# Kernel tuning notes

Measured on AMD Instinct MI355X. Metric: run time of the kernel, lower is better.

## Reference

```python
import jax, jax.numpy as jnp
import numpy as np

C = 20        # class_num
B = 2         # boxes per cell, N = B*5 + C = 30
S = 7         # grid size
NB = 16384    # batch
LAMBDA_COORD = 5.0
LAMBDA_NOOBJ = 0.5
OBJ_P = 0.2


def setup_inputs() -> dict:
    key = jax.random.key(0)
    ks = jax.random.split(key, 8)
    pred = jax.random.uniform(ks[0], (NB, S, S, B * 5 + C), jnp.float32)
    # object indicator per cell (target conf channel must be exactly 1 for obj cells)
    obj = (jax.random.uniform(ks[1], (NB, S, S, 1)) < OBJ_P).astype(jnp.float32)
    parts = []
    for b in range(B):
        xy = jax.random.uniform(ks[2 + 2 * b], (NB, S, S, 2), jnp.float32)
        wh = jax.random.uniform(ks[3 + 2 * b], (NB, S, S, 2), jnp.float32) * 0.9 + 0.05
        parts += [xy, wh, obj]
    cls = jax.random.uniform(ks[6], (NB, S, S, C), jnp.float32)
    target = jnp.concatenate(parts + [cls], axis=-1)
    return {"pred_tensor": pred, "target_tensor": target}


def _yolo_loss(pred, target):
    Nb, Sg, _, N = pred.shape
    Bb = (N - C) // 5
    dt = pred.dtype
    # grid[..., 0] = column (x offset), grid[..., 1] = row (y offset)
    gx, gy = jnp.meshgrid(jnp.arange(Sg), jnp.arange(Sg), indexing="xy")
    grid = jnp.stack([gx, gy], axis=-1).astype(dt)          # [S,S,2]

    pb = pred[..., : 5 * Bb].reshape(Nb, Sg, Sg, Bb, 5)      # raw pred boxes [Nb,S,S,B,5]
    tb0 = target[..., :5]                                    # raw gt box 0  [Nb,S,S,5]

    # txty -> absolute xy (normalized by S); wh stays raw
    pxy = (pb[..., :2] + grid[None, :, :, None, :]) / Sg
    pwh = pb[..., 2:4]
    gxy = (tb0[..., :2] + grid[None]) / Sg
    gwh = tb0[..., 2:4]

    # corners
    p1, p2 = pxy - 0.5 * pwh, pxy + 0.5 * pwh                # [Nb,S,S,B,2]
    g1 = (gxy - 0.5 * gwh)[..., None, :]                     # [Nb,S,S,1,2]
    g2 = (gxy + 0.5 * gwh)[..., None, :]

    # IoU of gt box against each of the B pred boxes, per cell
    wh = jnp.clip(jnp.minimum(g2, p2) - jnp.maximum(g1, p1), 0.0)
    inter = wh[..., 0] * wh[..., 1]                          # [Nb,S,S,B]
    area_p = pwh[..., 0] * pwh[..., 1]
    area_g = (gwh[..., 0] * gwh[..., 1])[..., None]
    iou = inter / (area_g + area_p - inter)

    best = jnp.argmax(iou, axis=-1)                          # [Nb,S,S]
    best_iou = jax.lax.stop_gradient(jnp.max(iou, axis=-1))  # .item() in torch detaches
    best_box = jnp.take_along_axis(pb, best[..., None, None], axis=3)[..., 0, :]  # raw [Nb,S,S,5]

    obj = target[..., 4] == 1.0
    objf = obj.astype(dt)
    noobjf = (target[..., 4] < 1.0).astype(dt)

    # coord losses (responsible box only)
    loss_xy = LAMBDA_COORD * jnp.sum(objf[..., None] * (best_box[..., :2] - tb0[..., :2]) ** 2)
    gwh_safe = jnp.where(obj[..., None], gwh, 1.0)           # keep sqrt grads finite under mask
    pwh_safe = jnp.where(obj[..., None], jnp.clip(best_box[..., 2:4], 0.0, 1.0), 1.0)
    loss_wh = LAMBDA_COORD * jnp.sum(objf[..., None] * (jnp.sqrt(pwh_safe) - jnp.sqrt(gwh_safe)) ** 2)

    loss_conf_posi = jnp.sum(objf * (best_box[..., 4] - best_iou) ** 2)
    loss_class = jnp.sum(objf[..., None] * (pred[..., 5 * Bb:] - target[..., 5 * Bb:]) ** 2)

    # negative conf: all B confs in no-obj cells + non-best confs in obj cells
    conf_all = pb[..., 4]                                    # [Nb,S,S,B]
    onehot = jax.nn.one_hot(best, Bb, dtype=dt)
    neg_w = objf[..., None] * (1.0 - onehot) + noobjf[..., None]
    loss_conf_nega = LAMBDA_NOOBJ * jnp.sum(neg_w * conf_all ** 2)

    total = loss_xy + loss_wh + loss_conf_posi + loss_conf_nega + loss_class
    bs = jnp.asarray(Nb, dt)
    return total / bs / bs  # original divides by batch_size twice


def reference(pred_tensor, target_tensor):
    return _yolo_loss(pred_tensor, target_tensor)
```

## Files before the change

kernel.cpp:

```cpp
#include <hip/hip_runtime.h>
#include <math.h>

constexpr int NCH = 30;
constexpr int CLS = 20;
constexpr int CPB = 256;
constexpr int NTHREADS = 256;

__global__ __launch_bounds__(NTHREADS) void yolo_loss_main(
    const float* __restrict__ pred, const float* __restrict__ targ,
    float* __restrict__ partial, int ncells)
{
  __shared__ float sp[CPB * NCH];
  __shared__ float st[CPB * NCH];
  __shared__ float swred[NTHREADS / 64];

  const int tid = threadIdx.x;
  const int cell0 = blockIdx.x * CPB;
  const int nc = min(CPB, ncells - cell0);
  const size_t base = (size_t)cell0 * NCH;

  if (nc == CPB) {
    const float4* gp = (const float4*)(pred + base);
    const float4* gt = (const float4*)(targ + base);
    float4* lp = (float4*)sp;
    float4* lt = (float4*)st;
    for (int i = tid; i < CPB * NCH / 4; i += NTHREADS) {
      lp[i] = gp[i];
      lt[i] = gt[i];
    }
  } else {
    int nfl = nc * NCH;
    for (int i = tid; i < nfl; i += NTHREADS) {
      sp[i] = pred[base + i];
      st[i] = targ[base + i];
    }
  }
  __syncthreads();

  float sum = 0.0f;
  if (tid < nc) {
    const float* p = sp + tid * NCH;
    const float* t = st + tid * NCH;
    int cellg = cell0 + tid;
    int rem = cellg % 49;
    int row = rem / 7;
    float fi = (float)row;
    float fj = (float)(rem - row * 7);

    float tx = t[0], ty = t[1], tw = t[2], th = t[3], tobj = t[4];
    float gx = (tx + fj) / 7.0f;
    float gy = (ty + fi) / 7.0f;
    float g1x = gx - 0.5f * tw, g1y = gy - 0.5f * th;
    float g2x = gx + 0.5f * tw, g2y = gy + 0.5f * th;
    float area_g = tw * th;

    float px0 = p[0], py0 = p[1], pw0 = p[2], ph0 = p[3], pc0 = p[4];
    float px1 = p[5], py1 = p[6], pw1 = p[7], ph1 = p[8], pc1 = p[9];

    float iou0, iou1;
    {
      float cx = (px0 + fj) / 7.0f, cy = (py0 + fi) / 7.0f;
      float wx = fminf(g2x, cx + 0.5f * pw0) - fmaxf(g1x, cx - 0.5f * pw0);
      float wy = fminf(g2y, cy + 0.5f * ph0) - fmaxf(g1y, cy - 0.5f * ph0);
      wx = fmaxf(wx, 0.0f); wy = fmaxf(wy, 0.0f);
      float inter = wx * wy;
      iou0 = inter / (area_g + pw0 * ph0 - inter);
    }
    {
      float cx = (px1 + fj) / 7.0f, cy = (py1 + fi) / 7.0f;
      float wx = fminf(g2x, cx + 0.5f * pw1) - fmaxf(g1x, cx - 0.5f * pw1);
      float wy = fminf(g2y, cy + 0.5f * ph1) - fmaxf(g1y, cy - 0.5f * ph1);
      wx = fmaxf(wx, 0.0f); wy = fmaxf(wy, 0.0f);
      float inter = wx * wy;
      iou1 = inter / (area_g + pw1 * ph1 - inter);
    }

    bool b1 = (iou1 > iou0);
    float biou = fmaxf(iou0, iou1);
    bool obj = (tobj == 1.0f);

    float lneg = 0.0f;
    if (!obj || b1)  lneg += pc0 * pc0;
    if (!obj || !b1) lneg += pc1 * pc1;
    sum = 0.5f * lneg;

    if (obj) {
      float bx = b1 ? px1 : px0;
      float by = b1 ? py1 : py0;
      float bw = b1 ? pw1 : pw0;
      float bh = b1 ? ph1 : ph0;
      float bc = b1 ? pc1 : pc0;
      float dx = bx - tx, dy = by - ty;
      sum += 5.0f * (dx * dx + dy * dy);
      float cw = fminf(fmaxf(bw, 0.0f), 1.0f);
      float chh = fminf(fmaxf(bh, 0.0f), 1.0f);
      float sw_ = sqrtf(cw) - sqrtf(tw);
      float sh_ = sqrtf(chh) - sqrtf(th);
      sum += 5.0f * (sw_ * sw_ + sh_ * sh_);
      float dc = bc - biou;
      sum += dc * dc;
      float lcls = 0.0f;
      #pragma unroll
      for (int k = 0; k < CLS; ++k) {
        float d = p[10 + k] - t[10 + k];
        lcls += d * d;
      }
      sum += lcls;
    }
  }

  #pragma unroll
  for (int off = 32; off > 0; off >>= 1) sum += __shfl_down(sum, off);
  if ((tid & 63) == 0) swred[tid >> 6] = sum;
  __syncthreads();
  if (tid == 0) {
    float s = 0.0f;
    #pragma unroll
    for (int w = 0; w < NTHREADS / 64; ++w) s += swred[w];
    partial[blockIdx.x] = s;
  }
}

__global__ __launch_bounds__(256) void yolo_loss_reduce(
    const float* __restrict__ partial, int n, float* __restrict__ out,
    float scale)
{
  __shared__ float swred[4];
  float s = 0.0f;
  for (int i = threadIdx.x; i < n; i += 256) s += partial[i];
  #pragma unroll
  for (int off = 32; off > 0; off >>= 1) s += __shfl_down(s, off);
  if ((threadIdx.x & 63) == 0) swred[threadIdx.x >> 6] = s;
  __syncthreads();
  if (threadIdx.x == 0)
    out[0] = (swred[0] + swred[1] + swred[2] + swred[3]) * scale;
}

extern "C" void kernel_launch(void* const* d_in, const int* in_sizes, int n_in,
                              void* d_out, int out_size, void* d_ws, size_t ws_size,
                              hipStream_t stream) {
  const float* pred = (const float*)d_in[0];
  const float* targ = (const float*)d_in[1];
  float* out = (float*)d_out;
  float* partial = (float*)d_ws;

  int total = in_sizes[0];
  int ncells = total / NCH;
  int nb = ncells / 49;
  int blocks = (ncells + CPB - 1) / CPB;
  float scale = 1.0f / ((float)nb * (float)nb);

  yolo_loss_main<<<blocks, NTHREADS, 0, stream>>>(pred, targ, partial, ncells);
  yolo_loss_reduce<<<1, 256, 0, stream>>>(partial, blocks, out, scale);
}
```

Before: 44.68 us.

## Compute class loss during coalesced load, stage only box channels in LDS

Measured after the change: 49.71 us. +11.3%, slower.

```diff
diff --git a/kernel.cpp b/kernel.cpp
--- a/kernel.cpp
+++ b/kernel.cpp
@@ -2,52 +2,89 @@
 #include <math.h>
 
 constexpr int NCH = 30;
-constexpr int CLS = 20;
 constexpr int CPB = 256;
-constexpr int NTHREADS = 256;
+constexpr int NT  = 256;
+constexpr int SPP = 11;
+constexpr int STP = 5;
 
-__global__ __launch_bounds__(NTHREADS) void yolo_loss_main(
+__global__ __launch_bounds__(NT, 4) void yolo_loss_main(
     const float* __restrict__ pred, const float* __restrict__ targ,
     float* __restrict__ partial, int ncells)
 {
-  __shared__ float sp[CPB * NCH];
-  __shared__ float st[CPB * NCH];
-  __shared__ float swred[NTHREADS / 64];
+  __shared__ float sp_box[CPB * SPP];
+  __shared__ float st_box[CPB * STP];
+  __shared__ float sobj[CPB];
+  __shared__ float swred[NT / 64];
 
   const int tid = threadIdx.x;
   const int cell0 = blockIdx.x * CPB;
   const int nc = min(CPB, ncells - cell0);
   const size_t base = (size_t)cell0 * NCH;
 
+  float csum = 0.0f;
+
   if (nc == CPB) {
+    float ov = targ[base + (size_t)tid * NCH + 4];
+    sobj[tid] = (ov == 1.0f) ? 1.0f : 0.0f;
+    __syncthreads();
+
     const float4* gp = (const float4*)(pred + base);
     const float4* gt = (const float4*)(targ + base);
-    float4* lp = (float4*)sp;
-    float4* lt = (float4*)st;
-    for (int i = tid; i < CPB * NCH / 4; i += NTHREADS) {
-      lp[i] = gp[i];
-      lt[i] = gt[i];
+    for (int f = tid; f < CPB * NCH / 4; f += NT) {
+      float4 pv = gp[f];
+      float4 tv = gt[f];
+      int d0 = 4 * f;
+      int cell = d0 / NCH;
+      int ch0 = d0 - cell * NCH;
+      float o = sobj[cell];
+      #pragma unroll
+      for (int j = 0; j < 4; ++j) {
+        int ch = ch0 + j;
+        int c = cell;
+        if (ch >= NCH) { ch -= NCH; c += 1; }
+        float pd = ((const float*)&pv)[j];
+        float td = ((const float*)&tv)[j];
+        if (ch >= 10) {
+          float dd = pd - td;
+          csum += o * dd * dd;
+        } else {
+          sp_box[c * SPP + ch] = pd;
+          if (ch < 4) st_box[c * STP + ch] = td;
+        }
+      }
     }
   } else {
-    int nfl = nc * NCH;
-    for (int i = tid; i < nfl; i += NTHREADS) {
-      sp[i] = pred[base + i];
-      st[i] = targ[base + i];
+    for (int i = tid; i < nc; i += NT) {
+      const float* p = pred + base + (size_t)i * NCH;
+      const float* t = targ + base + (size_t)i * NCH;
+      float o = (t[4] == 1.0f) ? 1.0f : 0.0f;
+      sobj[i] = o;
+      for (int k = 0; k < 10; ++k) sp_box[i * SPP + k] = p[k];
+      for (int k = 0; k < 4;  ++k) st_box[i * STP + k] = t[k];
+      for (int k = 10; k < NCH; ++k) {
+        float dd = p[k] - t[k];
+        csum += o * dd * dd;
+      }
     }
   }
   __syncthreads();
 
-  float sum = 0.0f;
+  float sum = csum;
   if (tid < nc) {
-    const float* p = sp + tid * NCH;
-    const float* t = st + tid * NCH;
+    const float* p = sp_box + tid * SPP;
     int cellg = cell0 + tid;
     int rem = cellg % 49;
     int row = rem / 7;
     float fi = (float)row;
     float fj = (float)(rem - row * 7);
 
-    float tx = t[0], ty = t[1], tw = t[2], th = t[3], tobj = t[4];
+    float tx = st_box[tid * STP + 0];
+    float ty = st_box[tid * STP + 1];
+    float tw = st_box[tid * STP + 2];
+    float th = st_box[tid * STP + 3];
+    float objf = sobj[tid];
+    bool obj = (objf != 0.0f);
+
     float gx = (tx + fj) / 7.0f;
     float gy = (ty + fi) / 7.0f;
     float g1x = gx - 0.5f * tw, g1y = gy - 0.5f * th;
@@ -77,12 +114,11 @@
 
     bool b1 = (iou1 > iou0);
     float biou = fmaxf(iou0, iou1);
-    bool obj = (tobj == 1.0f);
 
     float lneg = 0.0f;
     if (!obj || b1)  lneg += pc0 * pc0;
     if (!obj || !b1) lneg += pc1 * pc1;
-    sum = 0.5f * lneg;
+    sum += 0.5f * lneg;
 
     if (obj) {
       float bx = b1 ? px1 : px0;
@@ -92,20 +128,13 @@
       float bc = b1 ? pc1 : pc0;
       float dx = bx - tx, dy = by - ty;
       sum += 5.0f * (dx * dx + dy * dy);
-      float cw = fminf(fmaxf(bw, 0.0f), 1.0f);
+      float cw  = fminf(fmaxf(bw, 0.0f), 1.0f);
       float chh = fminf(fmaxf(bh, 0.0f), 1.0f);
-      float sw_ = sqrtf(cw) - sqrtf(tw);
+      float sw_ = sqrtf(cw)  - sqrtf(tw);
       float sh_ = sqrtf(chh) - sqrtf(th);
       sum += 5.0f * (sw_ * sw_ + sh_ * sh_);
       float dc = bc - biou;
       sum += dc * dc;
-      float lcls = 0.0f;
-      #pragma unroll
-      for (int k = 0; k < CLS; ++k) {
-        float d = p[10 + k] - t[10 + k];
-        lcls += d * d;
-      }
-      sum += lcls;
     }
   }
 
@@ -116,7 +145,7 @@
   if (tid == 0) {
     float s = 0.0f;
     #pragma unroll
-    for (int w = 0; w < NTHREADS / 64; ++w) s += swred[w];
+    for (int w = 0; w < NT / 64; ++w) s += swred[w];
     partial[blockIdx.x] = s;
   }
 }
@@ -150,6 +179,6 @@
   int blocks = (ncells + CPB - 1) / CPB;
   float scale = 1.0f / ((float)nb * (float)nb);
 
-  yolo_loss_main<<<blocks, NTHREADS, 0, stream>>>(pred, targ, partial, ncells);
+  yolo_loss_main<<<blocks, NT, 0, stream>>>(pred, targ, partial, ncells);
   yolo_loss_reduce<<<1, 256, 0, stream>>>(partial, blocks, out, scale);
 }
```
